# Performance work log

Hardware: AMD Instinct MI355X
Metric: run time of the kernel (lower is better)

Reference implementation:

```python
import jax, jax.numpy as jnp
import numpy as np
import math

N_SCALES = 8
WAVELET_LEN = 64
MIN_SCALE, MAX_SCALE = 1.0, 64.0
BATCH, SEQ, FEAT = 16, 4096, 64


def _morlet_init():
    # Faithful to _initialize_mother_wavelets
    t = np.linspace(-4.0, 4.0, WAVELET_LEN, dtype=np.float32)
    w = np.zeros((N_SCALES, WAVELET_LEN), dtype=np.float32)
    for i in range(N_SCALES):
        omega = 2.0 + i * 0.5
        sigma = 1.0 + i * 0.1
        wav = np.exp(-t ** 2 / (2 * sigma ** 2)) * np.cos(omega * t)
        w[i] = wav / np.linalg.norm(wav)
    return jnp.asarray(w)


def setup_inputs() -> dict:
    key = jax.random.key(0)
    k1, _ = jax.random.split(key)
    signal = jax.random.normal(k1, (BATCH, SEQ, FEAT), dtype=jnp.float32)
    mother_wavelets = _morlet_init()
    scale_weights = jnp.ones((N_SCALES,), dtype=jnp.float32)
    return {"signal": signal, "mother_wavelets": mother_wavelets, "scale_weights": scale_weights}


def _scales():
    return np.logspace(math.log10(MIN_SCALE), math.log10(MAX_SCALE), N_SCALES)


def _dilate(wavelet, scale):
    # F.interpolate(mode='linear', align_corners=True) to length int(WAVELET_LEN*scale)
    L_out = int(WAVELET_LEN * scale)
    if L_out > 1:
        pos = jnp.arange(L_out, dtype=jnp.float32) * ((WAVELET_LEN - 1) / (L_out - 1))
    else:
        pos = jnp.zeros((1,), dtype=jnp.float32)
    grid = jnp.arange(WAVELET_LEN, dtype=jnp.float32)
    return jnp.interp(pos, grid, wavelet) / math.sqrt(scale)


def reference(signal, mother_wavelets, scale_weights):
    # signal: (B, S, F) -> coefficients: (B, n_scales, S, F)
    B, S, F = signal.shape
    sig = jnp.swapaxes(signal, 1, 2)  # (B, F, S): batch all FFTs over b,f per scale
    scales = _scales()
    coeffs = []
    for i in range(N_SCALES):
        s = float(scales[i])
        w = _dilate(mother_wavelets[i], s)  # (L_dil,)
        n = S + w.shape[0] - 1
        n_fft = 2 ** int(math.ceil(math.log2(n)))
        Sf = jnp.fft.rfft(sig, n=n_fft, axis=-1)
        Wf = jnp.fft.rfft(w, n=n_fft)
        conv = jnp.fft.irfft(Sf * Wf, n=n_fft, axis=-1)[..., :S]  # (B, F, S)
        coeffs.append(conv)
    C = jnp.stack(coeffs, axis=1)            # (B, n_scales, F, S)
    C = jnp.swapaxes(C, 2, 3)                # (B, n_scales, S, F)
    return C * scale_weights[None, :, None, None]
```

## Files before the change

kernel.cpp:

```cpp
#include <hip/hip_runtime.h>
#include <hip/hip_bf16.h>
#include <math.h>

typedef __attribute__((ext_vector_type(8))) short bf16x8;
typedef __attribute__((ext_vector_type(4))) float f32x4;

#define NSC    8
#define SLEN   4096
#define FEAT   64
#define NQ     264
#define ATAB_B (NQ * 8 * 1024)

constexpr int L_[NSC]    = {64, 115, 210, 380, 689, 1248, 2261, 4096};
constexpr int CACT_[NSC] = {3, 5, 8, 13, 23, 40, 72, 129};

struct WavP { float step[NSC]; float isq[NSC]; };

__global__ void k_build_atab(const float* __restrict__ mw, const float* __restrict__ sw,
                             __hip_bfloat16* __restrict__ at, WavP wp)
{
  int e = blockIdx.x * 256 + threadIdx.x;
  int j = e & 7, l = (e >> 3) & 63, s = (e >> 9) & 7, q = e >> 12;
  int k = 16 * q - 32 + (l & 15) - 8 * (l >> 4) - j;
  float val = 0.f;
  if (k >= 0 && k < L_[s]) {
    float pos = (float)k * wp.step[s];
    int ii = (int)pos;
    float r;
    if (ii >= 63) r = mw[s * 64 + 63];
    else {
      float a = mw[s * 64 + ii];
      r = fmaf(pos - (float)ii, mw[s * 64 + ii + 1] - a, a);
    }
    val = r * wp.isq[s] * sw[s];
  }
  at[e] = __float2bfloat16(val);
}

__global__ __launch_bounds__(256) void k_transpose(const float* __restrict__ sig,
                                                   __hip_bfloat16* __restrict__ sigT2)
{
  __shared__ float t[4096];
  const int tid = threadIdx.x;
  const float* sp = sig + (size_t)blockIdx.x * 4096;
  for (int idx = tid; idx < 4096; idx += 256) {
    int r = idx >> 6, f = idx & 63;
    t[(r << 6) + (f ^ ((r & 7) << 3))] = sp[idx];
  }
  __syncthreads();
  __hip_bfloat16* op = sigT2 + (size_t)blockIdx.x * 4096;
  for (int e = tid; e < 4096; e += 256) {
    int h = e >> 11, n = (e >> 9) & 3, l = (e >> 3) & 63, i = e & 7;
    int f = n * 16 + (l & 15);
    int r = h * 32 + (l >> 4) * 8 + i;
    op[e] = __float2bfloat16(t[(r << 6) + (f ^ ((r & 7) << 3))]);
  }
}

template<int SB>
__device__ __forceinline__ void loadA4(const char* aw, int c_old, bf16x8* A) {
  #pragma unroll
  for (int i = 0; i < 4; ++i)
    if (c_old <= CACT_[SB + i])
      A[i] = *(const bf16x8*)(aw + (size_t)c_old * 16384 + (SB + i) * 1024);
}

template<int SB>
__device__ __forceinline__ void stepMFMA(int c_old, const bf16x8* A, const bf16x8* B,
                                         f32x4 (*acc)[4]) {
  __builtin_amdgcn_s_setprio(1);
  #pragma unroll
  for (int i = 3; i >= 0; --i) {
    if (c_old <= CACT_[SB + i]) {
      acc[i][0] = __builtin_amdgcn_mfma_f32_16x16x32_bf16(A[i], B[0], acc[i][0], 0, 0, 0);
      acc[i][1] = __builtin_amdgcn_mfma_f32_16x16x32_bf16(A[i], B[1], acc[i][1], 0, 0, 0);
      acc[i][2] = __builtin_amdgcn_mfma_f32_16x16x32_bf16(A[i], B[2], acc[i][2], 0, 0, 0);
      acc[i][3] = __builtin_amdgcn_mfma_f32_16x16x32_bf16(A[i], B[3], acc[i][3], 0, 0, 0);
    }
  }
  __builtin_amdgcn_s_setprio(0);
}

template<int SB>
__device__ __forceinline__ void run_pass(const char* aw, const char* sgb,
                                         short (*lbuf)[8192], int nsteps,
                                         int tid, int l, float* ob, int trow, int fl)
{
  f32x4 acc[4][4];
  const f32x4 z = {0.f, 0.f, 0.f, 0.f};
  #pragma unroll
  for (int i = 0; i < 4; ++i)
    #pragma unroll
    for (int n = 0; n < 4; ++n) acc[i][n] = z;

  const int nsc = (nsteps + 3) >> 2;

  auto stage = [&](int sc) {
    const char* gp = sgb - (size_t)(2 * sc + 1) * 8192 + tid * 16;
    char* lp = (char*)lbuf[sc & 1] + (tid >> 6) * 1024;
    #pragma unroll
    for (int it = 0; it < 4; ++it)
      __builtin_amdgcn_global_load_lds(
        (const __attribute__((address_space(1))) void*)(gp + it * 4096),
        (__attribute__((address_space(3))) void*)(lp + it * 4096), 16, 0, 0);
  };
  auto ldB = [&](int sc, int st, bf16x8* B) {
    const char* p = (const char*)lbuf[sc & 1] + (3 - (st & 3)) * 4096 + l * 16;
    #pragma unroll
    for (int n = 0; n < 4; ++n)
      B[n] = *(const bf16x8*)(p + n * 1024);
  };

  bf16x8 A0[4], A1[4], Ra[4], Rb[4];
  stage(0);
  loadA4<SB>(aw, 0, A0);
  loadA4<SB>(aw, 1, A1);
  __syncthreads();

  for (int sc = 0; sc < nsc; ++sc) {
    const int st = 4 * sc;
    if (sc + 1 < nsc) stage(sc + 1);
    ldB(sc, st, Ra);
    if (st + 1 < nsteps) ldB(sc, st + 1, Rb);
    stepMFMA<SB>(st, A0, Ra, acc);
    loadA4<SB>(aw, st + 2, A0);
    if (st + 2 < nsteps) ldB(sc, st + 2, Ra);
    if (st + 1 < nsteps) stepMFMA<SB>(st + 1, A1, Rb, acc);
    loadA4<SB>(aw, st + 3, A1);
    if (st + 3 < nsteps) ldB(sc, st + 3, Rb);
    if (st + 2 < nsteps) stepMFMA<SB>(st + 2, A0, Ra, acc);
    loadA4<SB>(aw, st + 4, A0);
    if (st + 3 < nsteps) stepMFMA<SB>(st + 3, A1, Rb, acc);
    loadA4<SB>(aw, st + 5, A1);
    __syncthreads();
  }

  #pragma unroll
  for (int i = 0; i < 4; ++i) {
    float* os = ob + (size_t)(SB + i) * SLEN * FEAT;
    #pragma unroll
    for (int n = 0; n < 4; ++n)
      #pragma unroll
      for (int r = 0; r < 4; ++r)
        os[(size_t)(trow + r) * FEAT + n * 16 + fl] = acc[i][n][r];
  }
}

__global__ __launch_bounds__(256, 3) void k_wavelet_mfma(
    const __hip_bfloat16* __restrict__ sigT2,
    const __hip_bfloat16* __restrict__ atab,
    float* __restrict__ out)
{
  __shared__ __align__(16) short lbuf[2][8192];

  const int tid = threadIdx.x;
  const int bid = blockIdx.x;
  const int tt  = 63 - (bid >> 4);
  const int b   = bid & 15;
  const int t0  = tt * 64;
  const int tw  = tid >> 6;
  const int l   = tid & 63;
  const int fl  = tid & 15;
  const int g   = (tid >> 4) & 3;

  const int C = tt + 1;
  const char* aw  = (const char*)atab + tw * 8192 + (size_t)l * 16;
  const char* sgb = (const char*)sigT2 + (size_t)(b * 64 + tt) * 8192;

  float* ob = out + (size_t)b * NSC * SLEN * FEAT;
  const int trow = t0 + tw * 16 + g * 4;

  run_pass<4>(aw, sgb, lbuf, 2 * C, tid, l, ob, trow, fl);
  run_pass<0>(aw, sgb, lbuf, min(2 * C, 14), tid, l, ob, trow, fl);
}

extern "C" void kernel_launch(void* const* d_in, const int* in_sizes, int n_in,
                              void* d_out, int out_size, void* d_ws, size_t ws_size,
                              hipStream_t stream) {
  const float* sig = (const float*)d_in[0];
  const float* mw  = (const float*)d_in[1];
  const float* sw  = (const float*)d_in[2];
  float*       out = (float*)d_out;

  __hip_bfloat16* atab  = (__hip_bfloat16*)d_ws;
  __hip_bfloat16* sigT2 = (__hip_bfloat16*)((char*)d_ws + 0x240000);

  WavP wp;
  const double lg = log10(64.0), st = lg / 7.0;
  for (int i = 0; i < NSC; ++i) {
    double y = (i == 7) ? lg : (double)i * st;
    double s = pow(10.0, y);
    wp.step[i] = (float)(63.0 / (double)(L_[i] - 1));
    wp.isq[i]  = (float)(1.0 / sqrt(s));
  }

  k_build_atab<<<NQ * 16, 256, 0, stream>>>(mw, sw, atab, wp);
  k_transpose<<<1024, 256, 0, stream>>>(sig, sigT2);
  k_wavelet_mfma<<<1024, 256, 0, stream>>>(sigT2, atab, out);
}
```

Before: 86.52 us.

## Balance MFMA work by pairing tiles and splitting scale passes across blocks

Result: slower. 127.2 us (+47.0%).

```diff
diff --git a/kernel.cpp b/kernel.cpp
--- a/kernel.cpp
+++ b/kernel.cpp
@@ -43,17 +43,31 @@
   __shared__ float t[4096];
   const int tid = threadIdx.x;
   const float* sp = sig + (size_t)blockIdx.x * 4096;
-  for (int idx = tid; idx < 4096; idx += 256) {
-    int r = idx >> 6, f = idx & 63;
-    t[(r << 6) + (f ^ ((r & 7) << 3))] = sp[idx];
+  #pragma unroll
+  for (int q2 = 0; q2 < 4; ++q2) {
+    int i4 = tid + 256 * q2;
+    float4 v = ((const float4*)sp)[i4];
+    int r = i4 >> 4, f0 = (i4 & 15) << 2;
+    #pragma unroll
+    for (int u = 0; u < 4; ++u)
+      t[(r << 6) + ((f0 + u) ^ ((r & 7) << 3))] = ((const float*)&v)[u];
   }
   __syncthreads();
   __hip_bfloat16* op = sigT2 + (size_t)blockIdx.x * 4096;
-  for (int e = tid; e < 4096; e += 256) {
-    int h = e >> 11, n = (e >> 9) & 3, l = (e >> 3) & 63, i = e & 7;
-    int f = n * 16 + (l & 15);
-    int r = h * 32 + (l >> 4) * 8 + i;
-    op[e] = __float2bfloat16(t[(r << 6) + (f ^ ((r & 7) << 3))]);
+  #pragma unroll
+  for (int w = 0; w < 2; ++w) {
+    const int e0 = tid * 16 + w * 8;
+    const int h = e0 >> 11, n = (e0 >> 9) & 3, ll = (e0 >> 3) & 63;
+    const int f = n * 16 + (ll & 15);
+    const int rb = h * 32 + ((ll >> 4) << 3);
+    bf16x8 o;
+    #pragma unroll
+    for (int u = 0; u < 8; ++u) {
+      int r = rb + u;
+      __hip_bfloat16 hb = __float2bfloat16(t[(r << 6) + (f ^ ((r & 7) << 3))]);
+      o[u] = *reinterpret_cast<short*>(&hb);
+    }
+    *(bf16x8*)(op + e0) = o;
   }
 }
 
@@ -111,7 +125,7 @@
       B[n] = *(const bf16x8*)(p + n * 1024);
   };
 
-  bf16x8 A0[4], A1[4], Ra[4], Rb[4];
+  bf16x8 A0[4], A1[4], B0[4], B1[4];
   stage(0);
   loadA4<SB>(aw, 0, A0);
   loadA4<SB>(aw, 1, A1);
@@ -120,17 +134,17 @@
   for (int sc = 0; sc < nsc; ++sc) {
     const int st = 4 * sc;
     if (sc + 1 < nsc) stage(sc + 1);
-    ldB(sc, st, Ra);
-    if (st + 1 < nsteps) ldB(sc, st + 1, Rb);
-    stepMFMA<SB>(st, A0, Ra, acc);
+    ldB(sc, st, B0);
+    if (st + 1 < nsteps) ldB(sc, st + 1, B1);
+    stepMFMA<SB>(st, A0, B0, acc);
     loadA4<SB>(aw, st + 2, A0);
-    if (st + 2 < nsteps) ldB(sc, st + 2, Ra);
-    if (st + 1 < nsteps) stepMFMA<SB>(st + 1, A1, Rb, acc);
+    if (st + 2 < nsteps) ldB(sc, st + 2, B0);
+    if (st + 1 < nsteps) stepMFMA<SB>(st + 1, A1, B1, acc);
     loadA4<SB>(aw, st + 3, A1);
-    if (st + 3 < nsteps) ldB(sc, st + 3, Rb);
-    if (st + 2 < nsteps) stepMFMA<SB>(st + 2, A0, Ra, acc);
+    if (st + 3 < nsteps) ldB(sc, st + 3, B1);
+    if (st + 2 < nsteps) stepMFMA<SB>(st + 2, A0, B0, acc);
     loadA4<SB>(aw, st + 4, A0);
-    if (st + 3 < nsteps) stepMFMA<SB>(st + 3, A1, Rb, acc);
+    if (st + 3 < nsteps) stepMFMA<SB>(st + 3, A1, B1, acc);
     loadA4<SB>(aw, st + 5, A1);
     __syncthreads();
   }
@@ -153,25 +167,29 @@
 {
   __shared__ __align__(16) short lbuf[2][8192];
 
-  const int tid = threadIdx.x;
-  const int bid = blockIdx.x;
-  const int tt  = 63 - (bid >> 4);
-  const int b   = bid & 15;
-  const int t0  = tt * 64;
-  const int tw  = tid >> 6;
-  const int l   = tid & 63;
-  const int fl  = tid & 15;
-  const int g   = (tid >> 4) & 3;
-
-  const int C = tt + 1;
-  const char* aw  = (const char*)atab + tw * 8192 + (size_t)l * 16;
-  const char* sgb = (const char*)sigT2 + (size_t)(b * 64 + tt) * 8192;
-
+  const int tid  = threadIdx.x;
+  const int p    = blockIdx.x >> 4;
+  const int b    = blockIdx.x & 15;
+  const int pass = blockIdx.y;
+  const int tw   = tid >> 6;
+  const int l    = tid & 63;
+  const int fl   = tid & 15;
+  const int g    = (tid >> 4) & 3;
+
+  const char* aw = (const char*)atab + tw * 8192 + (size_t)l * 16;
   float* ob = out + (size_t)b * NSC * SLEN * FEAT;
-  const int trow = t0 + tw * 16 + g * 4;
-
-  run_pass<4>(aw, sgb, lbuf, 2 * C, tid, l, ob, trow, fl);
-  run_pass<0>(aw, sgb, lbuf, min(2 * C, 14), tid, l, ob, trow, fl);
+
+  #pragma unroll
+  for (int which = 0; which < 2; ++which) {
+    const int tt = which ? p : 63 - p;
+    const int C  = tt + 1;
+    const char* sgb = (const char*)sigT2 + (size_t)(b * 64 + tt) * 8192;
+    const int trow  = tt * 64 + tw * 16 + g * 4;
+    if (pass == 0)
+      run_pass<4>(aw, sgb, lbuf, 2 * C, tid, l, ob, trow, fl);
+    else
+      run_pass<0>(aw, sgb, lbuf, min(2 * C, 14), tid, l, ob, trow, fl);
+  }
 }
 
 extern "C" void kernel_launch(void* const* d_in, const int* in_sizes, int n_in,
@@ -196,5 +214,5 @@
 
   k_build_atab<<<NQ * 16, 256, 0, stream>>>(mw, sw, atab, wp);
   k_transpose<<<1024, 256, 0, stream>>>(sig, sigT2);
-  k_wavelet_mfma<<<1024, 256, 0, stream>>>(sigT2, atab, out);
-}
+  k_wavelet_mfma<<<dim3(512, 2), 256, 0, stream>>>(sigT2, atab, out);
+}
```
